# Optimization experiments

Hardware: AMD Instinct MI355X
Metric: run time of the kernel (lower is better)

The kernel has to match this reference:

```python
import jax, jax.numpy as jnp
import numpy as np

D_MODEL = 256
NUM_HEADS = 8
DEPTH = D_MODEL // NUM_HEADS
CITY_SEQ = 2048
B = 4
SQ = 2048
EPS = 1e-9
WEIGHTING = 'IDW'  # branch used (Linear/IDW/Gaussian in original)


def setup_inputs() -> dict:
    key = jax.random.key(0)
    ks = jax.random.split(key, 12)
    s = 1.0 / np.sqrt(D_MODEL)
    return {
        'query': jax.random.normal(ks[0], (B, SQ, D_MODEL), jnp.float32),
        'values': jax.random.normal(ks[1], (B, SQ, D_MODEL), jnp.float32),
        'distance_matrix': jax.random.uniform(ks[2], (B, SQ, CITY_SEQ), jnp.float32),
        'Wq_w': jax.random.normal(ks[3], (D_MODEL, D_MODEL), jnp.float32) * s,
        'Wq_b': jnp.zeros((D_MODEL,), jnp.float32),
        'Wk_w': jax.random.normal(ks[4], (D_MODEL, D_MODEL), jnp.float32) * s,
        'Wk_b': jnp.zeros((D_MODEL,), jnp.float32),
        'Wv_w': jax.random.normal(ks[5], (D_MODEL, D_MODEL), jnp.float32) * s,
        'Wv_b': jnp.zeros((D_MODEL,), jnp.float32),
        'fc_w': jax.random.normal(ks[6], (D_MODEL, D_MODEL), jnp.float32) * s,
        'fc_b': jnp.zeros((D_MODEL,), jnp.float32),
        'trainable_keys': jax.random.normal(ks[7], (CITY_SEQ, D_MODEL), jnp.float32),
    }


def _distance_weights(dist):
    # IDW branch: per-row normalized inverse distance, shape [B, Sq, S]
    inv = 1.0 / (dist + EPS)
    return inv / jnp.sum(inv, axis=-1, keepdims=True)


def reference(query, values, distance_matrix, Wq_w, Wq_b, Wk_w, Wk_b,
              Wv_w, Wv_b, fc_w, fc_b, trainable_keys):
    b = query.shape[0]
    q = query @ Wq_w.T + Wq_b                      # [B, Sq, D]
    k = trainable_keys @ Wk_w.T + Wk_b             # [S, D] (shared across batch)
    v = values @ Wv_w.T + Wv_b                     # [B, S, D]

    qh = q.reshape(b, -1, NUM_HEADS, DEPTH)        # [B, Sq, H, d]
    kh = k.reshape(-1, NUM_HEADS, DEPTH)           # [S, H, d]
    vh = v.reshape(b, -1, NUM_HEADS, DEPTH)        # [B, S, H, d]

    scale = 1.0 / jnp.sqrt(jnp.asarray(DEPTH, jnp.float32))
    scores = jnp.einsum('bqhd,khd->bhqk', qh, kh) * scale   # [B, H, Sq, S]
    dw = _distance_weights(distance_matrix)[:, None, :, :]  # [B, 1, Sq, S]
    scores = scores * dw
    attn = jax.nn.softmax(scores, axis=-1)
    out = jnp.einsum('bhqk,bkhd->bqhd', attn, vh).reshape(b, -1, D_MODEL)
    return out @ fc_w.T + fc_b
```

## Files before the change

### kernel.cpp

```cpp
#include <hip/hip_runtime.h>

#define BB 4
#define SQn 2048
#define SS 2048
#define DM 256
#define DH 32

typedef unsigned short u16;
typedef unsigned int u32;
typedef _Float16 f16;
typedef __attribute__((ext_vector_type(8))) f16 f16x8;
typedef __attribute__((ext_vector_type(4))) f16 f16x4;
typedef __attribute__((ext_vector_type(8))) short s16x8;
typedef __attribute__((ext_vector_type(4))) float f32x4;
typedef __attribute__((ext_vector_type(2))) float f32x2;
typedef __attribute__((ext_vector_type(4))) u32 u32x4;
typedef __attribute__((ext_vector_type(2))) u32 u32x2;

__device__ __forceinline__ float bf2f(u16 x){ u32 u=((u32)x)<<16; return __builtin_bit_cast(float,u); }
__device__ __forceinline__ u16 f2bf(float f){ u32 u=__builtin_bit_cast(u32,f); u32 r=(u+0x7fffu+((u>>16)&1u))>>16; return (u16)r; }

__device__ __forceinline__ int detect_fl(const u32* __restrict__ q)
{
    u32 w = q[threadIdx.x & 63];
    u32 e = (w >> 7) & 0xFFu;
    int v = ((e >= 0x70u && e <= 0x85u) || ((w & 0xFFFFu) == 0u)) ? 1 : 0;
    unsigned long long b = __ballot(v);
    return (__popcll(b) >= 32) ? 0 : 1;
}

__device__ __forceinline__ f16x8 ld8(const void* p, size_t off, int fl)
{
    f16x8 r;
    if (fl) {
        const float* f = (const float*)p + off;
        f32x4 a = *(const f32x4*)f;
        f32x4 b = *(const f32x4*)(f + 4);
        #pragma unroll
        for (int i = 0; i < 4; ++i) { r[i] = (f16)a[i]; r[4+i] = (f16)b[i]; }
    } else {
        const u16* s = (const u16*)p + off;
        u32x4 v = *(const u32x4*)s;
        #pragma unroll
        for (int i = 0; i < 4; ++i) {
            u32 x = v[i];
            r[2*i]   = (f16)bf2f((u16)(x & 0xffff));
            r[2*i+1] = (f16)bf2f((u16)(x >> 16));
        }
    }
    return r;
}
__device__ __forceinline__ float ld1(const void* p, int idx, int fl)
{ return fl ? ((const float*)p)[idx] : bf2f(((const u16*)p)[idx]); }

__global__ __launch_bounds__(256) void mega_kernel(
    const void* __restrict__ query, const void* __restrict__ values, const void* __restrict__ tkeys,
    const void* __restrict__ Wq, const void* __restrict__ Wqb,
    const void* __restrict__ Wk, const void* __restrict__ Wkb,
    const void* __restrict__ Wv, const void* __restrict__ Wvb,
    const void* __restrict__ dist,
    f16* __restrict__ qf, f16* __restrict__ kf, u16* __restrict__ vt,
    u16* __restrict__ distT)
{
    __shared__ __align__(16) char sm[19968];
    int fl = detect_fl((const u32*)query);
    int x = blockIdx.x;
    int t = threadIdx.x;

    if (x < 1152) {
        int pbx = x >> 2, pby = x & 3;
        const void *X, *W, *Bi; int mode, rowbase;
        if (pbx < 128)      { X=query;  W=Wq; Bi=Wqb; mode=0; rowbase=pbx*64; }
        else if (pbx < 256) { X=values; W=Wv; Bi=Wvb; mode=2; rowbase=(pbx-128)*64; }
        else                { X=tkeys;  W=Wk; Bi=Wkb; mode=1; rowbase=(pbx-256)*64; }
        int colbase = pby * 64;

        f16 (*Xs)[40] = (f16(*)[40])sm;
        f16 (*Ws)[40] = (f16(*)[40])(sm + 5120);
        u16 (*Os)[72] = (u16(*)[72])(sm + 10240);

        int lane = t & 63, w = t >> 6;
        int quad = lane >> 4, l15 = lane & 15;

        const f32x4 fz = {0.f,0.f,0.f,0.f};
        f32x4 acc[4] = {fz,fz,fz,fz};

        for (int ks = 0; ks < 8; ++ks) {
            int k0 = ks * 32;
            {
                int row = t >> 2, ch = (t & 3) * 8;
                f16x8 xv = ld8(X, (size_t)(rowbase+row)*DM + k0 + ch, fl);
                f16x8 wv = ld8(W, (size_t)(colbase+row)*DM + k0 + ch, fl);
                *(f16x8*)(&Xs[row][ch]) = xv;
                *(f16x8*)(&Ws[row][ch]) = wv;
            }
            __syncthreads();
            f16x8 a = *(const f16x8*)(&Xs[w*16 + l15][quad*8]);
            #pragma unroll
            for (int nt = 0; nt < 4; ++nt) {
                f16x8 bfr = *(const f16x8*)(&Ws[nt*16 + l15][quad*8]);
                acc[nt] = __builtin_amdgcn_mfma_f32_16x16x32_f16(a, bfr, acc[nt], 0, 0, 0);
            }
            __syncthreads();
        }

        if (mode == 2) {
            int m = rowbase + w*16 + quad*4;
            int bb = m >> 11, s = m & 2047;
            int ktv = s >> 5, qv = (s >> 3) & 3, kk = s & 7;
            #pragma unroll
            for (int nt = 0; nt < 4; ++nt) {
                int col = colbase + nt*16 + l15;
                float bv = ld1(Bi, col, fl);
                int hv = col >> 5, ntv = (col >> 4) & 1;
                size_t idx = (((((size_t)(bb*8 + hv))*64 + ktv)*2 + ntv)*4 + qv)*128
                             + (size_t)(col & 15)*8 + kk;
                u32x2 pk;
                pk[0] = (u32)f2bf(acc[nt][0]+bv) | ((u32)f2bf(acc[nt][1]+bv) << 16);
                pk[1] = (u32)f2bf(acc[nt][2]+bv) | ((u32)f2bf(acc[nt][3]+bv) << 16);
                *(u32x2*)(vt + idx) = pk;
            }
        } else {
            #pragma unroll
            for (int nt = 0; nt < 4; ++nt) {
                int col = nt*16 + l15;
                float bv = ld1(Bi, colbase + col, fl);
                #pragma unroll
                for (int r = 0; r < 4; ++r)
                    Os[w*16 + quad*4 + r][col] = __builtin_bit_cast(u16, (f16)(acc[nt][r] + bv));
            }
            __syncthreads();
            #pragma unroll
            for (int p = 0; p < 2; ++p) {
                int rr = (t >> 3) + p*32;
                int ch = (t & 7) * 8;
                u32x4 v = *(const u32x4*)(&Os[rr][ch]);
                if (mode == 0) {
                    *(u32x4*)(qf + (size_t)(rowbase+rr)*DM + colbase + ch) = v;
                } else {
                    int head = (colbase + ch) >> 5;
                    int dh = ch & 31;
                    *(u32x4*)(kf + (size_t)head*(SS*DH) + (size_t)(rowbase+rr)*DH + dh) = v;
                }
            }
        }
    } else {
        int row = x - 1152;
        float* ps  = (float*)sm;
        float* srs = (float*)(sm + 16);

        float d[8];
        if (fl) {
            const float* p = (const float*)dist + (size_t)row * SS + t*8;
            f32x4 a = *(const f32x4*)p;
            f32x4 b4 = *(const f32x4*)(p + 4);
            #pragma unroll
            for (int i = 0; i < 4; ++i) { d[i] = a[i]; d[4+i] = b4[i]; }
        } else {
            const u16* p = (const u16*)dist + (size_t)row * SS + t*8;
            u32x4 v = *(const u32x4*)p;
            #pragma unroll
            for (int i = 0; i < 4; ++i) {
                u32 xw = v[i];
                d[2*i]   = bf2f((u16)(xw & 0xffff));
                d[2*i+1] = bf2f((u16)(xw >> 16));
            }
        }
        float s = 0.f;
        #pragma unroll
        for (int i = 0; i < 8; ++i) s += 1.0f / (d[i] + 1e-9f);
        #pragma unroll
        for (int dd = 1; dd < 64; dd <<= 1) s += __shfl_xor(s, dd);
        if ((t & 63) == 0) ps[t >> 6] = s;
        __syncthreads();
        if (t == 0) *srs = 0.17677669529663687f / (ps[0] + ps[1] + ps[2] + ps[3]);
        __syncthreads();
        float rs = *srs;

        int b = row >> 11, q = row & 2047;
        int qt = q >> 5, ql = q & 31;
        size_t base = ((size_t)((b*64 + qt)*64 + (t >> 2)))*1024 + ql*32 + (t & 3)*8;
        u32x4 pk;
        #pragma unroll
        for (int i = 0; i < 4; ++i) {
            u16 lo = __builtin_bit_cast(u16, (f16)(rs * __builtin_amdgcn_rcpf(d[2*i]   + 1e-9f)));
            u16 hi = __builtin_bit_cast(u16, (f16)(rs * __builtin_amdgcn_rcpf(d[2*i+1] + 1e-9f)));
            pk[i] = (u32)lo | ((u32)hi << 16);
        }
        *(u32x4*)(distT + base) = pk;
    }
}

#define LDP 40
#define LDO 264
#define DB_OFF 53248
#define OL_OFF  49152
#define OUTF_OFF 66048

__global__ __launch_bounds__(1024) void attn_kernel(
    const void* __restrict__ queryp,
    const u16* __restrict__ distT,
    const f16* __restrict__ qf, const f16* __restrict__ kf, const u16* __restrict__ vtg,
    const void* __restrict__ fcw, const void* __restrict__ fcb,
    void* __restrict__ out)
{
    __shared__ __align__(16) char smem[99840];

    int fl = detect_fl((const u32*)queryp);
    int t = threadIdx.x;
    int w = t >> 6, lane = t & 63;
    int quad = lane >> 4, l15 = lane & 15;
    int b = blockIdx.y, q0 = blockIdx.x * 32;
    int h = w & 7, khalf = w >> 3;

    u16* Pw = (u16*)(smem + w * 2560);
    u16* dbU = (u16*)(smem + DB_OFF);

    f16x8 aq[2];
    #pragma unroll
    for (int mt = 0; mt < 2; ++mt)
        aq[mt] = *(const f16x8*)(qf + (size_t)(b*SQn + q0 + mt*16 + l15)*DM + h*DH + quad*8);

    u32 ov = (l15 == 0) ? 0x3F803F80u : 0u;
    u32x4 ovv = {ov, ov, ov, ov};
    s16x8 ones = __builtin_bit_cast(s16x8, ovv);

    const f32x4 fz = {0.f,0.f,0.f,0.f};
    f32x4 o[2][2] = {{fz,fz},{fz,fz}};
    f32x4 lacc[2] = {fz, fz};

    const f16* kfh = kf + (size_t)h * (SS*DH);
    const u16* vth = vtg + (((size_t)(b*8 + h)) << 16);
    const u16* dTb = distT + ((size_t)(b*64 + blockIdx.x))*64*1024;

    int g  = t >> 9;
    int tt = t & 511;
    int drow = tt >> 4, dcol = (tt & 15)*2;

    {
        u32 sv = *(const u32*)(dTb + (size_t)(g*32)*1024 + tt*2);
        *(u32*)(dbU + g*1152 + drow*36 + dcol) = sv;
    }
    f16x8 ck[2]; s16x8 cv[2];
    {
        int ktg0 = khalf * 32;
        #pragma unroll
        for (int nt = 0; nt < 2; ++nt) {
            ck[nt] = *(const f16x8*)(kfh + (size_t)(ktg0*32 + nt*16 + l15)*DH + quad*8);
            cv[nt] = __builtin_bit_cast(s16x8,
                *(const u32x4*)(vth + (size_t)ktg0*1024 + nt*512 + quad*128 + l15*8));
        }
    }
    __syncthreads();

    for (int kt = 0; kt < 32; ++kt) {
        int ktn  = (kt + 1) & 31;
        int ktgn = khalf*32 + ktn;

        u32 sv = *(const u32*)(dTb + (size_t)(g*32 + ktn)*1024 + tt*2);
        f16x8 nk[2]; s16x8 nv[2];
        #pragma unroll
        for (int nt = 0; nt < 2; ++nt) {
            nk[nt] = *(const f16x8*)(kfh + (size_t)(ktgn*32 + nt*16 + l15)*DH + quad*8);
            nv[nt] = __builtin_bit_cast(s16x8,
                *(const u32x4*)(vth + (size_t)ktgn*1024 + nt*512 + quad*128 + l15*8));
        }

        const u16* dbc = dbU + ((kt & 1)*2 + khalf)*1152;
        f16x4 ddh[2][2];
        #pragma unroll
        for (int mt = 0; mt < 2; ++mt)
            #pragma unroll
            for (int nt = 0; nt < 2; ++nt)
                ddh[mt][nt] = *(const f16x4*)(dbc + (mt*16 + l15)*36 + nt*16 + quad*4);

        f32x4 st[2][2];
        #pragma unroll
        for (int mt = 0; mt < 2; ++mt)
            #pragma unroll
            for (int nt = 0; nt < 2; ++nt)
                st[mt][nt] = __builtin_amdgcn_mfma_f32_16x16x32_f16(ck[nt], aq[mt], fz, 0, 0, 0);

        #pragma unroll
        for (int mt = 0; mt < 2; ++mt)
            #pragma unroll
            for (int nt = 0; nt < 2; ++nt) {
                u32 pb[4];
                #pragma unroll
                for (int r = 0; r < 4; ++r) {
                    float p = __expf(st[mt][nt][r] * (float)ddh[mt][nt][r]);
                    pb[r] = __builtin_bit_cast(u32, p);
                }
                u32x2 pk;
                pk[0] = __builtin_amdgcn_perm(pb[1], pb[0], 0x07060302u);
                pk[1] = __builtin_amdgcn_perm(pb[3], pb[2], 0x07060302u);
                *(u32x2*)(Pw + (mt*16 + l15)*LDP + nt*16 + quad*4) = pk;
            }
        __asm__ __volatile__("" ::: "memory");

        #pragma unroll
        for (int mt = 0; mt < 2; ++mt) {
            s16x8 ap = *(const s16x8*)(Pw + (mt*16 + l15)*LDP + quad*8);
            lacc[mt] = __builtin_amdgcn_mfma_f32_16x16x32_bf16(ap, ones, lacc[mt], 0, 0, 0);
            #pragma unroll
            for (int nt = 0; nt < 2; ++nt)
                o[mt][nt] = __builtin_amdgcn_mfma_f32_16x16x32_bf16(ap, cv[nt], o[mt][nt], 0, 0, 0);
        }

        *(u32*)(dbU + (((kt + 1) & 1)*2 + g)*1152 + drow*36 + dcol) = sv;
        __syncthreads();

        ck[0] = nk[0]; ck[1] = nk[1]; cv[0] = nv[0]; cv[1] = nv[1];
    }

    float* Cx = (float*)smem;
    if (w >= 8) {
        float* dst = Cx + ((w - 8)*64 + lane)*24;
        *(f32x4*)(dst +  0) = o[0][0];
        *(f32x4*)(dst +  4) = o[0][1];
        *(f32x4*)(dst +  8) = o[1][0];
        *(f32x4*)(dst + 12) = o[1][1];
        *(f32x4*)(dst + 16) = lacc[0];
        *(f32x4*)(dst + 20) = lacc[1];
    }
    __syncthreads();
    f16* Ol = (f16*)(smem + OL_OFF);
    if (w < 8) {
        const float* src = Cx + (w*64 + lane)*24;
        o[0][0] += *(const f32x4*)(src +  0);
        o[0][1] += *(const f32x4*)(src +  4);
        o[1][0] += *(const f32x4*)(src +  8);
        o[1][1] += *(const f32x4*)(src + 12);
        lacc[0] += *(const f32x4*)(src + 16);
        lacc[1] += *(const f32x4*)(src + 20);

        #pragma unroll
        for (int mt = 0; mt < 2; ++mt)
            #pragma unroll
            for (int r = 0; r < 4; ++r) {
                float lv = __shfl(lacc[mt][r], lane & 48);
                float inv = 1.0f / lv;
                o[mt][0][r] *= inv;
                o[mt][1][r] *= inv;
            }

        #pragma unroll
        for (int mt = 0; mt < 2; ++mt)
            #pragma unroll
            for (int nt = 0; nt < 2; ++nt)
                #pragma unroll
                for (int r = 0; r < 4; ++r)
                    Ol[(mt*16 + quad*4 + r)*LDO + h*DH + nt*16 + l15] = (f16)o[mt][nt][r];
    }
    __syncthreads();

    f32x4 c[2] = {fz, fz};
    int n = w*16 + l15;
    for (int ks = 0; ks < 8; ++ks) {
        f16x8 bw = ld8(fcw, (size_t)n*DM + ks*32 + quad*8, fl);
        #pragma unroll
        for (int mt = 0; mt < 2; ++mt) {
            f16x8 a2 = *(const f16x8*)(Ol + (mt*16 + l15)*LDO + ks*32 + quad*8);
            c[mt] = __builtin_amdgcn_mfma_f32_16x16x32_f16(a2, bw, c[mt], 0, 0, 0);
        }
    }
    float* OutF = (float*)(smem + OUTF_OFF);
    {
        float bv = ld1(fcb, n, fl);
        #pragma unroll
        for (int mt = 0; mt < 2; ++mt)
            #pragma unroll
            for (int r = 0; r < 4; ++r)
                OutF[(mt*16 + quad*4 + r)*LDO + n] = c[mt][r] + bv;
    }
    __syncthreads();
    if (fl) {
        float* of = (float*)out;
        int row = t >> 5, col = (t & 31) * 8;
        f32x4 v0 = *(const f32x4*)(OutF + row*LDO + col);
        f32x4 v1 = *(const f32x4*)(OutF + row*LDO + col + 4);
        float* dst = of + ((size_t)(b*SQn + q0 + row))*DM + col;
        *(f32x4*)dst       = v0;
        *(f32x4*)(dst + 4) = v1;
    } else {
        u16* ob = (u16*)out;
        int row = t >> 5, col = (t & 31) * 8;
        f32x4 v0 = *(const f32x4*)(OutF + row*LDO + col);
        f32x4 v1 = *(const f32x4*)(OutF + row*LDO + col + 4);
        u32x4 pk;
        pk[0] = (u32)f2bf(v0[0]) | ((u32)f2bf(v0[1]) << 16);
        pk[1] = (u32)f2bf(v0[2]) | ((u32)f2bf(v0[3]) << 16);
        pk[2] = (u32)f2bf(v1[0]) | ((u32)f2bf(v1[1]) << 16);
        pk[3] = (u32)f2bf(v1[2]) | ((u32)f2bf(v1[3]) << 16);
        *(u32x4*)(ob + ((size_t)(b*SQn + q0 + row))*DM + col) = pk;
    }
}

extern "C" void kernel_launch(void* const* d_in, const int* in_sizes, int n_in,
                              void* d_out, int out_size, void* d_ws, size_t ws_size,
                              hipStream_t stream)
{
    const void* query  = d_in[0];
    const void* values = d_in[1];
    const void* dist   = d_in[2];
    const void* Wq     = d_in[3];
    const void* Wqb    = d_in[4];
    const void* Wk     = d_in[5];
    const void* Wkb    = d_in[6];
    const void* Wv     = d_in[7];
    const void* Wvb    = d_in[8];
    const void* fcw    = d_in[9];
    const void* fcb    = d_in[10];
    const void* tkeys  = d_in[11];

    char* ws   = (char*)d_ws;
    f16*  qf   = (f16*)ws;
    f16*  kf   = (f16*)(ws + (4u << 20));
    u16*  vt   = (u16*)(ws + (5u << 20));
    u16*  dT   = (u16*)(ws + (16u << 20));

    mega_kernel<<<dim3(1152 + BB*SQn), 256, 0, stream>>>(
        query, values, tkeys, Wq, Wqb, Wk, Wkb, Wv, Wvb, dist, qf, kf, vt, dT);
    attn_kernel<<<dim3(64, 4), 1024, 0, stream>>>(query, dT, qf, kf, vt, fcw, fcb, d_out);
}
```

Measured before the change: 191.7 us.

## Store distance weights in MFMA fragment order and drop LDS staging in attention

The distance preprocessing now runs one block per (batch, 32-query tile). It reduces the row sums first, then writes the normalized fp16 weights already permuted into the per-lane MFMA output fragment layout, staging the data through a per-wave LDS transpose. The attention kernel then loads each lane's 16 weights straight from global memory with two vector loads and prefetches them into registers one step ahead. This removes the shared-memory double buffer and the per-iteration __syncthreads from the main loop. In exchange the preprocessing reads the distance matrix twice and launches far fewer, heavier blocks, which may reduce its parallelism.

```diff
diff --git a/kernel.cpp b/kernel.cpp
--- a/kernel.cpp
+++ b/kernel.cpp
@@ -66,6 +66,8 @@
     int fl = detect_fl((const u32*)query);
     int x = blockIdx.x;
     int t = threadIdx.x;
+    int lane = t & 63, w = t >> 6;
+    int quad = lane >> 4, l15 = lane & 15;
 
     if (x < 1152) {
         int pbx = x >> 2, pby = x & 3;
@@ -78,9 +80,6 @@
         f16 (*Xs)[40] = (f16(*)[40])sm;
         f16 (*Ws)[40] = (f16(*)[40])(sm + 5120);
         u16 (*Os)[72] = (u16(*)[72])(sm + 10240);
-
-        int lane = t & 63, w = t >> 6;
-        int quad = lane >> 4, l15 = lane & 15;
 
         const f32x4 fz = {0.f,0.f,0.f,0.f};
         f32x4 acc[4] = {fz,fz,fz,fz};
@@ -145,55 +144,104 @@
             }
         }
     } else {
-        int row = x - 1152;
-        float* ps  = (float*)sm;
-        float* srs = (float*)(sm + 16);
-
-        float d[8];
-        if (fl) {
-            const float* p = (const float*)dist + (size_t)row * SS + t*8;
-            f32x4 a = *(const f32x4*)p;
-            f32x4 b4 = *(const f32x4*)(p + 4);
-            #pragma unroll
-            for (int i = 0; i < 4; ++i) { d[i] = a[i]; d[4+i] = b4[i]; }
-        } else {
-            const u16* p = (const u16*)dist + (size_t)row * SS + t*8;
-            u32x4 v = *(const u32x4*)p;
-            #pragma unroll
-            for (int i = 0; i < 4; ++i) {
-                u32 xw = v[i];
-                d[2*i]   = bf2f((u16)(xw & 0xffff));
-                d[2*i+1] = bf2f((u16)(xw >> 16));
-            }
-        }
-        float s = 0.f;
-        #pragma unroll
-        for (int i = 0; i < 8; ++i) s += 1.0f / (d[i] + 1e-9f);
-        #pragma unroll
-        for (int dd = 1; dd < 64; dd <<= 1) s += __shfl_xor(s, dd);
-        if ((t & 63) == 0) ps[t >> 6] = s;
+        int bid = x - 1152;
+        int b = bid >> 6, qt = bid & 63;
+        float* rsv   = (float*)sm;
+        float* tileB = (float*)(sm + 128);
+
+        {
+            int q = t >> 3, c = t & 7;
+            size_t rowoff = (size_t)(b*SQn + qt*32 + q) * SS;
+            float s = 0.f;
+            if (fl) {
+                const float* p = (const float*)dist + rowoff + c*8;
+                for (int i = 0; i < 32; ++i) {
+                    f32x4 a  = *(const f32x4*)(p + i*64);
+                    f32x4 b4 = *(const f32x4*)(p + i*64 + 4);
+                    #pragma unroll
+                    for (int j = 0; j < 4; ++j) {
+                        s += __builtin_amdgcn_rcpf(a[j]  + 1e-9f);
+                        s += __builtin_amdgcn_rcpf(b4[j] + 1e-9f);
+                    }
+                }
+            } else {
+                const u16* p = (const u16*)dist + rowoff + c*8;
+                for (int i = 0; i < 32; ++i) {
+                    u32x4 v = *(const u32x4*)(p + i*64);
+                    #pragma unroll
+                    for (int j = 0; j < 4; ++j) {
+                        u32 xw = v[j];
+                        s += __builtin_amdgcn_rcpf(bf2f((u16)(xw & 0xffff)) + 1e-9f);
+                        s += __builtin_amdgcn_rcpf(bf2f((u16)(xw >> 16))    + 1e-9f);
+                    }
+                }
+            }
+            #pragma unroll
+            for (int d = 1; d < 8; d <<= 1) s += __shfl_xor(s, d);
+            if ((t & 7) == 0) rsv[t >> 3] = 0.17677669529663687f / s;
+        }
         __syncthreads();
-        if (t == 0) *srs = 0.17677669529663687f / (ps[0] + ps[1] + ps[2] + ps[3]);
-        __syncthreads();
-        float rs = *srs;
-
-        int b = row >> 11, q = row & 2047;
-        int qt = q >> 5, ql = q & 31;
-        size_t base = ((size_t)((b*64 + qt)*64 + (t >> 2)))*1024 + ql*32 + (t & 3)*8;
-        u32x4 pk;
-        #pragma unroll
-        for (int i = 0; i < 4; ++i) {
-            u16 lo = __builtin_bit_cast(u16, (f16)(rs * __builtin_amdgcn_rcpf(d[2*i]   + 1e-9f)));
-            u16 hi = __builtin_bit_cast(u16, (f16)(rs * __builtin_amdgcn_rcpf(d[2*i+1] + 1e-9f)));
-            pk[i] = (u32)lo | ((u32)hi << 16);
-        }
-        *(u32x4*)(distT + base) = pk;
+
+        float* tw = tileB + w*1152;
+        u16* dTp = distT + ((size_t)(b*64 + qt))*65536;
+        for (int ii = 0; ii < 16; ++ii) {
+            int kt = w*16 + ii;
+            {
+                int q2 = lane >> 1, h = lane & 1;
+                size_t off = (size_t)(b*SQn + qt*32 + q2)*SS + kt*32 + h*16;
+                float vals[16];
+                if (fl) {
+                    const float* p = (const float*)dist + off;
+                    #pragma unroll
+                    for (int j4 = 0; j4 < 4; ++j4) {
+                        f32x4 v = *(const f32x4*)(p + j4*4);
+                        #pragma unroll
+                        for (int j = 0; j < 4; ++j) vals[j4*4+j] = v[j];
+                    }
+                } else {
+                    const u16* p = (const u16*)dist + off;
+                    u32x4 v0 = *(const u32x4*)p;
+                    u32x4 v1 = *(const u32x4*)(p + 8);
+                    #pragma unroll
+                    for (int j = 0; j < 4; ++j) {
+                        vals[2*j]   = bf2f((u16)(v0[j] & 0xffff));
+                        vals[2*j+1] = bf2f((u16)(v0[j] >> 16));
+                        vals[8+2*j]   = bf2f((u16)(v1[j] & 0xffff));
+                        vals[8+2*j+1] = bf2f((u16)(v1[j] >> 16));
+                    }
+                }
+                #pragma unroll
+                for (int j4 = 0; j4 < 4; ++j4) {
+                    f32x4 v = {vals[j4*4], vals[j4*4+1], vals[j4*4+2], vals[j4*4+3]};
+                    *(f32x4*)(tw + q2*36 + h*16 + j4*4) = v;
+                }
+            }
+            u32 pk[8];
+            #pragma unroll
+            for (int mt = 0; mt < 2; ++mt) {
+                float rsq = rsv[mt*16 + l15];
+                #pragma unroll
+                for (int nt = 0; nt < 2; ++nt) {
+                    f32x4 dv = *(const f32x4*)(tw + (mt*16 + l15)*36 + nt*16 + quad*4);
+                    u16 h0 = __builtin_bit_cast(u16, (f16)(rsq * __builtin_amdgcn_rcpf(dv[0] + 1e-9f)));
+                    u16 h1 = __builtin_bit_cast(u16, (f16)(rsq * __builtin_amdgcn_rcpf(dv[1] + 1e-9f)));
+                    u16 h2 = __builtin_bit_cast(u16, (f16)(rsq * __builtin_amdgcn_rcpf(dv[2] + 1e-9f)));
+                    u16 h3 = __builtin_bit_cast(u16, (f16)(rsq * __builtin_amdgcn_rcpf(dv[3] + 1e-9f)));
+                    pk[(mt*2+nt)*2]   = (u32)h0 | ((u32)h1 << 16);
+                    pk[(mt*2+nt)*2+1] = (u32)h2 | ((u32)h3 << 16);
+                }
+            }
+            u16* dst = dTp + (size_t)kt*1024 + lane*16;
+            u32x4 s0 = {pk[0], pk[1], pk[2], pk[3]};
+            u32x4 s1 = {pk[4], pk[5], pk[6], pk[7]};
+            *(u32x4*)dst       = s0;
+            *(u32x4*)(dst + 8) = s1;
+        }
     }
 }
 
 #define LDP 40
 #define LDO 264
-#define DB_OFF 53248
 #define OL_OFF  49152
 #define OUTF_OFF 66048
 
@@ -214,7 +262,6 @@
     int h = w & 7, khalf = w >> 3;
 
     u16* Pw = (u16*)(smem + w * 2560);
-    u16* dbU = (u16*)(smem + DB_OFF);
 
     f16x8 aq[2];
     #pragma unroll
@@ -231,17 +278,9 @@
 
     const f16* kfh = kf + (size_t)h * (SS*DH);
     const u16* vth = vtg + (((size_t)(b*8 + h)) << 16);
-    const u16* dTb = distT + ((size_t)(b*64 + blockIdx.x))*64*1024;
-
-    int g  = t >> 9;
-    int tt = t & 511;
-    int drow = tt >> 4, dcol = (tt & 15)*2;
-
-    {
-        u32 sv = *(const u32*)(dTb + (size_t)(g*32)*1024 + tt*2);
-        *(u32*)(dbU + g*1152 + drow*36 + dcol) = sv;
-    }
-    f16x8 ck[2]; s16x8 cv[2];
+    const u16* dTb = distT + ((size_t)(b*64 + blockIdx.x))*65536;
+
+    f16x8 ck[2]; s16x8 cv[2]; f16x8 cd0, cd1;
     {
         int ktg0 = khalf * 32;
         #pragma unroll
@@ -250,14 +289,14 @@
             cv[nt] = __builtin_bit_cast(s16x8,
                 *(const u32x4*)(vth + (size_t)ktg0*1024 + nt*512 + quad*128 + l15*8));
         }
-    }
-    __syncthreads();
+        cd0 = *(const f16x8*)(dTb + (size_t)ktg0*1024 + lane*16);
+        cd1 = *(const f16x8*)(dTb + (size_t)ktg0*1024 + lane*16 + 8);
+    }
 
     for (int kt = 0; kt < 32; ++kt) {
         int ktn  = (kt + 1) & 31;
         int ktgn = khalf*32 + ktn;
 
-        u32 sv = *(const u32*)(dTb + (size_t)(g*32 + ktn)*1024 + tt*2);
         f16x8 nk[2]; s16x8 nv[2];
         #pragma unroll
         for (int nt = 0; nt < 2; ++nt) {
@@ -265,14 +304,8 @@
             nv[nt] = __builtin_bit_cast(s16x8,
                 *(const u32x4*)(vth + (size_t)ktgn*1024 + nt*512 + quad*128 + l15*8));
         }
-
-        const u16* dbc = dbU + ((kt & 1)*2 + khalf)*1152;
-        f16x4 ddh[2][2];
-        #pragma unroll
-        for (int mt = 0; mt < 2; ++mt)
-            #pragma unroll
-            for (int nt = 0; nt < 2; ++nt)
-                ddh[mt][nt] = *(const f16x4*)(dbc + (mt*16 + l15)*36 + nt*16 + quad*4);
+        f16x8 nd0 = *(const f16x8*)(dTb + (size_t)ktgn*1024 + lane*16);
+        f16x8 nd1 = *(const f16x8*)(dTb + (size_t)ktgn*1024 + lane*16 + 8);
 
         f32x4 st[2][2];
         #pragma unroll
@@ -288,7 +321,8 @@
                 u32 pb[4];
                 #pragma unroll
                 for (int r = 0; r < 4; ++r) {
-                    float p = __expf(st[mt][nt][r] * (float)ddh[mt][nt][r]);
+                    float dv = (float)(mt == 0 ? cd0[nt*4 + r] : cd1[nt*4 + r]);
+                    float p = __expf(st[mt][nt][r] * dv);
                     pb[r] = __builtin_bit_cast(u32, p);
                 }
                 u32x2 pk;
@@ -307,12 +341,11 @@
                 o[mt][nt] = __builtin_amdgcn_mfma_f32_16x16x32_bf16(ap, cv[nt], o[mt][nt], 0, 0, 0);
         }
 
-        *(u32*)(dbU + (((kt + 1) & 1)*2 + g)*1152 + drow*36 + dcol) = sv;
-        __syncthreads();
-
         ck[0] = nk[0]; ck[1] = nk[1]; cv[0] = nv[0]; cv[1] = nv[1];
-    }
-
+        cd0 = nd0; cd1 = nd1;
+    }
+
+    __syncthreads();
     float* Cx = (float*)smem;
     if (w >= 8) {
         float* dst = Cx + ((w - 8)*64 + lane)*24;
@@ -419,7 +452,7 @@
     u16*  vt   = (u16*)(ws + (5u << 20));
     u16*  dT   = (u16*)(ws + (16u << 20));
 
-    mega_kernel<<<dim3(1152 + BB*SQn), 256, 0, stream>>>(
+    mega_kernel<<<dim3(1152 + 256), 256, 0, stream>>>(
         query, values, tkeys, Wq, Wqb, Wk, Wkb, Wv, Wvb, dist, qf, kf, vt, dT);
     attn_kernel<<<dim3(64, 4), 1024, 0, stream>>>(query, dT, qf, kf, vt, fcw, fcb, d_out);
 }
```

After: 198.9 us. 1.04x slower.
